# Kernel tuning notes

Measured on AMD Instinct MI355X. Metric: run time of the kernel, lower is better.

Reference implementation:

```python
import jax, jax.numpy as jnp
import numpy as np
import math
from jax import lax

S = 2048   # layer_size (number of neurons)
T = 384    # timesteps per forward call
ALPHA = 0.15
DT = 0.1
THRESH = -50.0
V_RESET = -70.0
VL = -70.0
GL = 0.025
CM = 0.5
TAU = CM / GL                                   # 20.0
COEF = DT ** ALPHA * math.gamma(2.0 - ALPHA) / CM  # dt^alpha * Gamma(2-alpha) / Cm


def setup_inputs() -> dict:
    key = jax.random.key(0)
    I_old = jax.random.normal(key, (S, T), dtype=jnp.float32)
    # class-level fractional (Grunwald-Letnikov style) weight vector, x=5000
    x = 5000
    nv = np.arange(x - 1)
    w = ((x - nv + 1) ** (1.0 - ALPHA) - (x - nv) ** (1.0 - ALPHA)).astype(np.float32)
    return {"I_old": I_old, "weights": jnp.asarray(w)}


def _forward(I_old, weights):
    S_, T_ = I_old.shape
    dtype = I_old.dtype
    # wr[a] = weights[-a]: the memory weight applied to a delta that is `a` steps old.
    # Original: np.inner(weights[-N+1:], delta_trace) pairs oldest delta with weights[-(N-1)]
    # and the newest delta with weights[-1].
    wr = jnp.concatenate([jnp.zeros((1,), dtype), weights[::-1][:T_].astype(dtype)])  # [T+1]
    jidx = jnp.arange(T_)  # buffer slot j holds the delta appended at global step j

    def step(carry, xs):
        V, buf = carry          # V: [S], buf: [S, T] delta history (slot j = delta of step j)
        n, I_n = xs             # n: scalar step index, I_n: [S]
        # fractional memory term: sum_{j=1}^{n-1} wr[n-j] * delta_j
        ages = n - jidx                                        # [T]
        coeff = jnp.where((ages >= 1) & (jidx >= 1),
                          wr[jnp.clip(ages, 0, T_)], jnp.zeros((), dtype))  # [T]
        memory = buf @ coeff                                   # [S]
        # three update rules depending on the global step counter
        V1 = V + (DT / TAU) * (-V + I_n / GL)                  # N == 1 branch
        V2 = COEF * (-GL * (V - VL) + I_n) + V - memory        # N >= 2 branch
        V_pre = jnp.where(n == 0, jnp.full_like(V, -70.0),
                          jnp.where(n == 1, V1, V2))
        spike = (V - THRESH > 0).astype(dtype)                 # spike uses PREVIOUS V
        reset = lax.stop_gradient(spike * (THRESH - V_RESET))  # detached reset
        V_new = V_pre - reset
        buf = buf.at[:, n].set(V_new - V)                      # append delta (n=0 slot masked out)
        return (V_new, buf), (spike, V_new)

    V0 = jnp.zeros((S_,), dtype)          # V_trace initialized to 0 per neuron
    buf0 = jnp.zeros((S_, T_), dtype)
    (_, _), (spk, trc) = lax.scan(step, (V0, buf0), (jnp.arange(T_), I_old.T))
    return spk.T, trc.T                    # each [S, T]


def reference(I_old, weights):
    return _forward(I_old, weights)
```

## Files before the change

kernel.cpp:

```cpp
#include <hip/hip_runtime.h>
#include <cmath>

#define T_STEPS 384
#define CH 64
#define NCH 6
#define WS 392

typedef float v2f __attribute__((ext_vector_type(2)));
typedef float v4f __attribute__((ext_vector_type(4)));

__device__ __forceinline__ float readlane_f(float v, int l) {
    return __int_as_float(__builtin_amdgcn_readlane(__float_as_int(v), l));
}
__device__ __forceinline__ float wave_shr1_f(float v) {
    return __int_as_float(__builtin_amdgcn_mov_dpp(__float_as_int(v), 0x138, 0xf, 0xf, true));
}
template<int CTRL, int RM>
__device__ __forceinline__ float dpp0_f(float v) {
    return __int_as_float(__builtin_amdgcn_update_dpp(0, __float_as_int(v), CTRL, RM, 0xf, true));
}
__device__ __forceinline__ float wave_iscan_add(float v) {
    v += dpp0_f<0x111, 0xf>(v);
    v += dpp0_f<0x112, 0xf>(v);
    v += dpp0_f<0x114, 0xf>(v);
    v += dpp0_f<0x118, 0xf>(v);
    v += dpp0_f<0x142, 0xa>(v);
    v += dpp0_f<0x143, 0xc>(v);
    return v;
}

__global__ __launch_bounds__(128, 4)
void flif_kernel(const float* __restrict__ I_old, const float* __restrict__ W,
                 float* __restrict__ out, float cm1, float c2, float c3, int Stot)
{
    const int tid  = threadIdx.x;
    const int wid  = tid >> 6;
    const int lane = tid & 63;
    const int s    = blockIdx.x;

    __shared__ __align__(16) float wtr[4 * WS];
    __shared__ __align__(16) float dbuf[T_STEPS];
    __shared__ float accs[2][CH];

    for (int k = tid; k < 4 * WS; k += 128) {
        const int r = k / WS, kk = k - r * WS;
        const int i = (kk ^ 1) + r;
        wtr[k] = (i <= 382) ? W[4998 - i] : 0.0f;
    }
    ((float*)accs)[tid] = 0.0f;
    __syncthreads();

    const int rl = lane & 3;
    const float* wlp = wtr + rl * WS + (lane - rl);

    if (wid == 1) {
        v4f wc2[16];
        #pragma unroll
        for (int j = 0; j < 16; ++j)
            wc2[j] = *reinterpret_cast<const v4f*>(wlp + 64 + 4 * j);

        v2f A2a = {0.f,0.f}, A2b = {0.f,0.f}, A3a = {0.f,0.f}, A3b = {0.f,0.f};
        v2f A4a = {0.f,0.f}, A4b = {0.f,0.f}, A5a = {0.f,0.f}, A5b = {0.f,0.f};
        #pragma unroll
        for (int c = 0; c < NCH; ++c) {
            if (c >= 1 && c <= 4) {
                const int src = c - 1;
                const float* dp = dbuf + src * CH;
                #pragma unroll
                for (int k = 0; k <= 60; k += 4) {
                    const v4f d4 = *reinterpret_cast<const v4f*>(dp + k);
                    #pragma unroll
                    for (int t = c + 1; t <= 5; ++t) {
                        const int g = t - src;
                        const v4f w4 = (g == 2) ? wc2[(60 - k) >> 2]
                            : *reinterpret_cast<const v4f*>(wlp + (g * 64 - k - 4));
                        v2f& Aa = (t == 2) ? A2a : (t == 3) ? A3a : (t == 4) ? A4a : A5a;
                        v2f& Ab = (t == 2) ? A2b : (t == 3) ? A3b : (t == 4) ? A4b : A5b;
                        Aa = d4.xy * w4.zw + Aa;
                        Ab = d4.zw * w4.xy + Ab;
                    }
                }
                const v2f hv = (c == 1) ? (A2a + A2b) : (c == 2) ? (A3a + A3b)
                             : (c == 3) ? (A4a + A4b) : (A5a + A5b);
                accs[(c + 1) & 1][lane] = hv.x + hv.y;
            }
            __syncthreads();
        }
        return;
    }

    v4f wc1[16];
    #pragma unroll
    for (int j = 0; j < 16; ++j)
        wc1[j] = *reinterpret_cast<const v4f*>(wlp + 4 * j);

    const float* Irow = I_old + (size_t)s * T_STEPS;
    float Inext = Irow[lane];
    const float w0seed = (lane >= 1) ? W[4999 - lane] : 0.0f;
    const float wr1n = -W[4998];
    const float b1 = cm1 - W[4998];
    const float b2 = cm1 - W[4997];
    const float w2seed = (lane >= 1) ? (cm1 - W[4999 - lane]) : 0.0f;

    float Vcs = 0.0f;
    float rvprev = 0.0f;
    float tcs[NCH], spks[NCH];

    for (int c = 0; c < NCH; ++c) {
        const int cb = c * CH;
        const float Ic = Inext;
        if (c + 1 < NCH) Inext = Irow[cb + CH + lane];

        float acc = (c == 0) ? 0.0f : accs[c & 1][lane];
        if (c >= 1) {
            const float* dp = dbuf + (c - 1) * CH;
            v2f a2 = {0.0f, 0.0f}, a3 = {0.0f, 0.0f};
            #pragma unroll
            for (int m0 = 60; m0 >= 0; m0 -= 4) {
                const v4f d4 = *reinterpret_cast<const v4f*>(dp + (60 - m0));
                const v4f w4 = wc1[m0 >> 2];
                a2 = d4.xy * w4.zw + a2;
                a3 = d4.zw * w4.xy + a3;
            }
            acc += (a2.x + a2.y) + (a3.x + a3.y);
        }

        const float u0 = fmaf(c3, Ic, c2) - acc;
        const float Vs = Vcs;
        float tc;
        float Vend;

        {
            float u, Pq0, Pq1, w2;
            float dm1 = 0.0f, dm2 = 0.0f;
            if (c == 0) {
                const float V0 = -90.0f;
                const float wf = wave_shr1_f(w0seed);
                const float I1 = readlane_f(Ic, 1);
                const float V1 = fmaf(0.005f, (I1 / 0.025f) - V0, V0);
                const float d1 = V1 - V0;
                const float ue = fmaf(-wf, d1, u0);
                u = fmaf(cm1, V1, ue);
                *reinterpret_cast<float2*>(&dbuf[0]) = make_float2(0.0f, d1);
                Pq0 = readlane_f(u, 2);
                Pq1 = readlane_f(u, 3);
                w2 = wave_shr1_f(wave_shr1_f(w2seed));
                #pragma unroll
                for (int i = 2; i < CH; ++i) {
                    const float x  = fmaf(b2, dm2, (i & 1) ? Pq1 : Pq0);
                    const float dn = fmaf(b1, dm1, x);
                    const float nf = readlane_f(u, (i + 2) & 63);
                    if (i & 1) Pq1 = nf; else Pq0 = nf;
                    u = fmaf(w2, dn, u);
                    w2 = wave_shr1_f(w2);
                    if (i & 1)
                        *reinterpret_cast<float2*>(&dbuf[i - 1]) = make_float2(dm1, dn);
                    dm2 = dm1; dm1 = dn;
                }
                const float dl = dbuf[lane];
                tc = -90.0f + wave_iscan_add(dl);
                Vend = readlane_f(tc, 63);
            } else {
                u = fmaf(cm1, Vcs, u0);
                Pq0 = readlane_f(u, 0) + rvprev;
                Pq1 = readlane_f(u, 1);
                w2 = w2seed;
                #pragma unroll
                for (int i = 0; i < CH; ++i) {
                    const float x  = fmaf(b2, dm2, (i & 1) ? Pq1 : Pq0);
                    const float dn = fmaf(b1, dm1, x);
                    const float nf = readlane_f(u, (i + 2) & 63);
                    if (i & 1) Pq1 = nf; else Pq0 = nf;
                    u = fmaf(w2, dn, u);
                    w2 = wave_shr1_f(w2);
                    if (i & 1)
                        *reinterpret_cast<float2*>(&dbuf[cb + i - 1]) = make_float2(dm1, dn);
                    dm2 = dm1; dm1 = dn;
                }
                const float dl = dbuf[cb + lane];
                tc = Vcs + wave_iscan_add(dl);
                Vend = readlane_f(tc, 63);
            }
        }

        bool replayed = false;
        if (__any(tc > -50.5f)) {
            replayed = true;
            float V, d, b, P, w;
            float tcf = 0.0f;
            float uf = u0;
            if (c == 0) {
                V = -90.0f;
                if (lane == 0) tcf = V;
                w = wave_shr1_f(w0seed);
                const float I1 = readlane_f(Ic, 1);
                const float V1 = fmaf(0.005f, (I1 / 0.025f) - V, V);
                const float d1 = V1 - V;
                P = readlane_f(uf, 2);
                uf = fmaf(-w, d1, uf);
                w = wave_shr1_f(w);
                if (lane == 1) tcf = V1;
                V = V1; d = d1;
                b = fmaf(cm1, V, (V > -50.0f) ? -20.0f : 0.0f);
                #pragma unroll
                for (int i = 2; i < CH; ++i) {
                    const float t = fmaf(wr1n, d, P);
                    d = t + b;
                    P = readlane_f(uf, (i + 1) & 63);
                    V = V + d;
                    const float rv = (V > -50.0f) ? -20.0f : 0.0f;
                    b = fmaf(cm1, V, rv);
                    uf = fmaf(-w, d, uf);
                    w = wave_shr1_f(w);
                    tcf = (lane == i) ? V : tcf;
                }
            } else {
                V = Vcs; d = 0.0f;
                b = fmaf(cm1, Vcs, rvprev);
                w = w0seed;
                P = readlane_f(uf, 0);
                #pragma unroll
                for (int i = 0; i < CH; ++i) {
                    const float t = fmaf(wr1n, d, P);
                    d = t + b;
                    P = readlane_f(uf, (i + 1) & 63);
                    V = V + d;
                    const float rv = (V > -50.0f) ? -20.0f : 0.0f;
                    b = fmaf(cm1, V, rv);
                    uf = fmaf(-w, d, uf);
                    w = wave_shr1_f(w);
                    tcf = (lane == i) ? V : tcf;
                }
            }
            tc = tcf; Vend = V;
        }
        rvprev = (Vend > -50.0f) ? -20.0f : 0.0f;

        float prev = __shfl_up(tc, 1);
        if (lane == 0) prev = Vs;
        spks[c] = (prev > -50.0f) ? 1.0f : 0.0f;
        if (replayed) {
            float dd = tc - prev;
            if (c == 0 && lane == 0) dd = 0.0f;
            dbuf[cb + lane] = dd;
        }
        tcs[c] = tc;
        Vcs = Vend;
        __syncthreads();
    }

    float* out_spk = out + (size_t)s * T_STEPS;
    float* out_trc = out + (size_t)Stot * T_STEPS + (size_t)s * T_STEPS;
    #pragma unroll
    for (int c = 0; c < NCH; ++c) {
        out_spk[c * CH + lane] = spks[c];
        out_trc[c * CH + lane] = tcs[c];
    }
}

extern "C" void kernel_launch(void* const* d_in, const int* in_sizes, int n_in,
                              void* d_out, int out_size, void* d_ws, size_t ws_size,
                              hipStream_t stream) {
    const float* I = (const float*)d_in[0];
    const float* W = (const float*)d_in[1];
    float* out = (float*)d_out;
    const int S = in_sizes[0] / T_STEPS;

    const double COEF = std::pow(0.1, 0.15) * std::tgamma(1.85) / 0.5;
    const float c3  = (float)COEF;
    const float cm1 = (float)(-COEF * 0.025);
    const float c2  = (float)(COEF * 0.025 * -70.0);

    flif_kernel<<<S, 128, 0, stream>>>(I, W, out, cm1, c2, c3, S);
}
```

Measured before the change: 72.87 us.

## Process two neurons per block, one per wave, removing helper-wave split

Previously each block handled one neuron, with a second wave precomputing the older-chunk memory contributions and handing them over through shared memory with per-chunk barriers. Now each wave independently handles its own neuron and computes the full history convolution itself. This halves the number of blocks, removes all in-loop __syncthreads, and writes outputs per chunk instead of buffering them in registers. In exchange each wave does more serial FMA work per chunk, and the launch-bounds occupancy hint is lowered from 4 to 2.

```diff
diff --git a/kernel.cpp b/kernel.cpp
--- a/kernel.cpp
+++ b/kernel.cpp
@@ -29,65 +29,29 @@
     return v;
 }
 
-__global__ __launch_bounds__(128, 4)
+__global__ __launch_bounds__(128, 2)
 void flif_kernel(const float* __restrict__ I_old, const float* __restrict__ W,
                  float* __restrict__ out, float cm1, float c2, float c3, int Stot)
 {
     const int tid  = threadIdx.x;
     const int wid  = tid >> 6;
     const int lane = tid & 63;
-    const int s    = blockIdx.x;
+    const int s    = (blockIdx.x << 1) + wid;
 
     __shared__ __align__(16) float wtr[4 * WS];
-    __shared__ __align__(16) float dbuf[T_STEPS];
-    __shared__ float accs[2][CH];
+    __shared__ __align__(16) float dbuf2[2][T_STEPS];
 
     for (int k = tid; k < 4 * WS; k += 128) {
         const int r = k / WS, kk = k - r * WS;
         const int i = (kk ^ 1) + r;
         wtr[k] = (i <= 382) ? W[4998 - i] : 0.0f;
     }
-    ((float*)accs)[tid] = 0.0f;
     __syncthreads();
-
+    if (s >= Stot) return;
+
+    float* dbw = dbuf2[wid];
     const int rl = lane & 3;
     const float* wlp = wtr + rl * WS + (lane - rl);
-
-    if (wid == 1) {
-        v4f wc2[16];
-        #pragma unroll
-        for (int j = 0; j < 16; ++j)
-            wc2[j] = *reinterpret_cast<const v4f*>(wlp + 64 + 4 * j);
-
-        v2f A2a = {0.f,0.f}, A2b = {0.f,0.f}, A3a = {0.f,0.f}, A3b = {0.f,0.f};
-        v2f A4a = {0.f,0.f}, A4b = {0.f,0.f}, A5a = {0.f,0.f}, A5b = {0.f,0.f};
-        #pragma unroll
-        for (int c = 0; c < NCH; ++c) {
-            if (c >= 1 && c <= 4) {
-                const int src = c - 1;
-                const float* dp = dbuf + src * CH;
-                #pragma unroll
-                for (int k = 0; k <= 60; k += 4) {
-                    const v4f d4 = *reinterpret_cast<const v4f*>(dp + k);
-                    #pragma unroll
-                    for (int t = c + 1; t <= 5; ++t) {
-                        const int g = t - src;
-                        const v4f w4 = (g == 2) ? wc2[(60 - k) >> 2]
-                            : *reinterpret_cast<const v4f*>(wlp + (g * 64 - k - 4));
-                        v2f& Aa = (t == 2) ? A2a : (t == 3) ? A3a : (t == 4) ? A4a : A5a;
-                        v2f& Ab = (t == 2) ? A2b : (t == 3) ? A3b : (t == 4) ? A4b : A5b;
-                        Aa = d4.xy * w4.zw + Aa;
-                        Ab = d4.zw * w4.xy + Ab;
-                    }
-                }
-                const v2f hv = (c == 1) ? (A2a + A2b) : (c == 2) ? (A3a + A3b)
-                             : (c == 3) ? (A4a + A4b) : (A5a + A5b);
-                accs[(c + 1) & 1][lane] = hv.x + hv.y;
-            }
-            __syncthreads();
-        }
-        return;
-    }
 
     v4f wc1[16];
     #pragma unroll
@@ -102,27 +66,42 @@
     const float b2 = cm1 - W[4997];
     const float w2seed = (lane >= 1) ? (cm1 - W[4999 - lane]) : 0.0f;
 
+    float* out_spk = out + (size_t)s * T_STEPS;
+    float* out_trc = out + (size_t)Stot * T_STEPS + (size_t)s * T_STEPS;
+
     float Vcs = 0.0f;
     float rvprev = 0.0f;
-    float tcs[NCH], spks[NCH];
 
     for (int c = 0; c < NCH; ++c) {
         const int cb = c * CH;
         const float Ic = Inext;
         if (c + 1 < NCH) Inext = Irow[cb + CH + lane];
 
-        float acc = (c == 0) ? 0.0f : accs[c & 1][lane];
+        float acc = 0.0f;
         if (c >= 1) {
-            const float* dp = dbuf + (c - 1) * CH;
             v2f a2 = {0.0f, 0.0f}, a3 = {0.0f, 0.0f};
-            #pragma unroll
-            for (int m0 = 60; m0 >= 0; m0 -= 4) {
-                const v4f d4 = *reinterpret_cast<const v4f*>(dp + (60 - m0));
-                const v4f w4 = wc1[m0 >> 2];
-                a2 = d4.xy * w4.zw + a2;
-                a3 = d4.zw * w4.xy + a3;
-            }
-            acc += (a2.x + a2.y) + (a3.x + a3.y);
+            for (int src = 0; src + 1 < c; ++src) {
+                const float* dp = dbw + src * CH;
+                const float* wp = wlp + (c - src) * 64;
+                #pragma unroll
+                for (int k = 0; k <= 60; k += 4) {
+                    const v4f d4 = *reinterpret_cast<const v4f*>(dp + k);
+                    const v4f w4 = *reinterpret_cast<const v4f*>(wp - k - 4);
+                    a2 = d4.xy * w4.zw + a2;
+                    a3 = d4.zw * w4.xy + a3;
+                }
+            }
+            {
+                const float* dp = dbw + (c - 1) * CH;
+                #pragma unroll
+                for (int m0 = 60; m0 >= 0; m0 -= 4) {
+                    const v4f d4 = *reinterpret_cast<const v4f*>(dp + (60 - m0));
+                    const v4f w4 = wc1[m0 >> 2];
+                    a2 = d4.xy * w4.zw + a2;
+                    a3 = d4.zw * w4.xy + a3;
+                }
+            }
+            acc = (a2.x + a2.y) + (a3.x + a3.y);
         }
 
         const float u0 = fmaf(c3, Ic, c2) - acc;
@@ -141,7 +120,7 @@
                 const float d1 = V1 - V0;
                 const float ue = fmaf(-wf, d1, u0);
                 u = fmaf(cm1, V1, ue);
-                *reinterpret_cast<float2*>(&dbuf[0]) = make_float2(0.0f, d1);
+                *reinterpret_cast<float2*>(&dbw[0]) = make_float2(0.0f, d1);
                 Pq0 = readlane_f(u, 2);
                 Pq1 = readlane_f(u, 3);
                 w2 = wave_shr1_f(wave_shr1_f(w2seed));
@@ -154,10 +133,10 @@
                     u = fmaf(w2, dn, u);
                     w2 = wave_shr1_f(w2);
                     if (i & 1)
-                        *reinterpret_cast<float2*>(&dbuf[i - 1]) = make_float2(dm1, dn);
+                        *reinterpret_cast<float2*>(&dbw[i - 1]) = make_float2(dm1, dn);
                     dm2 = dm1; dm1 = dn;
                 }
-                const float dl = dbuf[lane];
+                const float dl = dbw[lane];
                 tc = -90.0f + wave_iscan_add(dl);
                 Vend = readlane_f(tc, 63);
             } else {
@@ -174,10 +153,10 @@
                     u = fmaf(w2, dn, u);
                     w2 = wave_shr1_f(w2);
                     if (i & 1)
-                        *reinterpret_cast<float2*>(&dbuf[cb + i - 1]) = make_float2(dm1, dn);
+                        *reinterpret_cast<float2*>(&dbw[cb + i - 1]) = make_float2(dm1, dn);
                     dm2 = dm1; dm1 = dn;
                 }
-                const float dl = dbuf[cb + lane];
+                const float dl = dbw[cb + lane];
                 tc = Vcs + wave_iscan_add(dl);
                 Vend = readlane_f(tc, 63);
             }
@@ -238,23 +217,14 @@
 
         float prev = __shfl_up(tc, 1);
         if (lane == 0) prev = Vs;
-        spks[c] = (prev > -50.0f) ? 1.0f : 0.0f;
+        out_spk[cb + lane] = (prev > -50.0f) ? 1.0f : 0.0f;
+        out_trc[cb + lane] = tc;
         if (replayed) {
             float dd = tc - prev;
             if (c == 0 && lane == 0) dd = 0.0f;
-            dbuf[cb + lane] = dd;
-        }
-        tcs[c] = tc;
+            dbw[cb + lane] = dd;
+        }
         Vcs = Vend;
-        __syncthreads();
-    }
-
-    float* out_spk = out + (size_t)s * T_STEPS;
-    float* out_trc = out + (size_t)Stot * T_STEPS + (size_t)s * T_STEPS;
-    #pragma unroll
-    for (int c = 0; c < NCH; ++c) {
-        out_spk[c * CH + lane] = spks[c];
-        out_trc[c * CH + lane] = tcs[c];
     }
 }
 
@@ -271,5 +241,5 @@
     const float cm1 = (float)(-COEF * 0.025);
     const float c2  = (float)(COEF * 0.025 * -70.0);
 
-    flif_kernel<<<S, 128, 0, stream>>>(I, W, out, cm1, c2, c3, S);
-}
+    flif_kernel<<<(S + 1) / 2, 128, 0, stream>>>(I, W, out, cm1, c2, c3, S);
+}
```

Result: slower. 76.08 us (+4.4%).
